# Performance work log

Hardware: AMD Instinct MI355X
Metric: run time of the kernel (lower is better)

Reference implementation:

```python
import jax, jax.numpy as jnp
import numpy as np

N = 100000          # nodes
E = 1600000         # edges (avg degree 16)
IN_DIM = 32
HID = 64
K = 2
XH = IN_DIM + HID   # 96, DiffConv input dim


def _xavier(key, shape):
    fan_in, fan_out = shape[-2], shape[-1]
    lim = float(np.sqrt(6.0 / (fan_in + fan_out)))
    return jax.random.uniform(key, shape, jnp.float32, -lim, lim)


def setup_inputs() -> dict:
    key = jax.random.key(0)
    ks = jax.random.split(key, 8)
    x = jax.random.normal(ks[0], (N, IN_DIM), jnp.float32)
    h = jax.random.normal(ks[1], (N, HID), jnp.float32)
    edge_index = jax.random.randint(ks[2], (2, E), 0, N, dtype=jnp.int32)
    edge_weight = jax.random.uniform(ks[3], (E,), jnp.float32)
    # stacked per-hop linear weights for each gate: (K+1, XH, HID)
    Wr = _xavier(ks[4], (K + 1, XH, HID))
    Wz = _xavier(ks[5], (K + 1, XH, HID))
    Wc = _xavier(ks[6], (K + 1, XH, HID))
    br = jnp.zeros((HID,), jnp.float32)
    bz = jnp.zeros((HID,), jnp.float32)
    bc = jnp.zeros((HID,), jnp.float32)
    return {"x": x, "h": h, "edge_index": edge_index, "edge_weight": edge_weight,
            "Wr": Wr, "br": br, "Wz": Wz, "bz": bz, "Wc": Wc, "bc": bc}


def _diff_conv(x, src, dst, norm_w, W, b, n):
    # DC(X) = sum_k Linear_k(P^k X),  P = D^{-1} W (row-normalised)
    out = x @ W[0]
    x_k = x
    for k in range(1, W.shape[0]):
        msgs = norm_w[:, None] * x_k[src]                     # gather + scale (E, F)
        x_k = jax.ops.segment_sum(msgs, dst, num_segments=n)  # scatter-add (N, F)
        out = out + x_k @ W[k]
    return out + b


def reference(x, h, edge_index, edge_weight, Wr, br, Wz, bz, Wc, bc):
    n = x.shape[0]
    src, dst = edge_index[0], edge_index[1]
    # out-degree normalisation on source nodes (clamped at 1)
    out_deg = jax.ops.segment_sum(jnp.ones_like(edge_weight), src, num_segments=n)
    out_deg = jnp.maximum(out_deg, 1.0)
    norm_w = edge_weight / out_deg[src]
    xh = jnp.concatenate([x, h], axis=-1)
    r = jax.nn.sigmoid(_diff_conv(xh, src, dst, norm_w, Wr, br, n))
    z = jax.nn.sigmoid(_diff_conv(xh, src, dst, norm_w, Wz, bz, n))
    xrh = jnp.concatenate([x, r * h], axis=-1)
    c = jnp.tanh(_diff_conv(xrh, src, dst, norm_w, Wc, bc, n))
    return z * h + (1.0 - z) * c
```

## Files before the change

### kernel.cpp

```cpp
#include <hip/hip_runtime.h>
#include <math.h>

#define NN 100000
#define NE 1600000
#define ECAP 64
#define GN 64
#define WSTR 296
#define LSTR 104

#define EPB 4096
#define NBLKA 391
#define BINB 256
#define NBINS 391
#define BCAP 4736

typedef __attribute__((ext_vector_type(4))) float f32x4;
typedef __attribute__((ext_vector_type(8))) short s16x8;

__device__ __forceinline__ unsigned int bfbits(float v) {
  unsigned int b = __float_as_uint(v);
  b += 0x7fffu + ((b >> 16) & 1u);
  return b >> 16;
}
__device__ __forceinline__ float bflo(unsigned int v) { return __uint_as_float(v << 16); }
__device__ __forceinline__ float bfhi(unsigned int v) { return __uint_as_float(v & 0xffff0000u); }
__device__ __forceinline__ float bf1(unsigned short v) { return __uint_as_float((unsigned int)v << 16); }

__global__ __launch_bounds__(256) void k_binA(const int* __restrict__ src,
                                              const int* __restrict__ dst,
                                              const float* __restrict__ ew,
                                              int* __restrict__ gcur1,
                                              int* __restrict__ gcur2,
                                              int2* __restrict__ rec1,
                                              unsigned char* __restrict__ rec2) {
  __shared__ int h1[NBINS], h2[NBINS];
  int tid = threadIdx.x;
  for (int t = tid; t < NBINS; t += 256) { h1[t] = 0; h2[t] = 0; }
  __syncthreads();
  int base = blockIdx.x * EPB;
  int end = base + EPB; if (end > NE) end = NE;
  for (int e = base + tid; e < end; e += 256) {
    atomicAdd(&h1[dst[e] >> 8], 1);
    atomicAdd(&h2[src[e] >> 8], 1);
  }
  __syncthreads();
  for (int t = tid; t < NBINS; t += 256) {
    int c1 = h1[t];
    h1[t] = t * BCAP + (c1 ? atomicAdd(&gcur1[t], c1) : 0);
    int c2 = h2[t];
    h2[t] = t * BCAP + (c2 ? atomicAdd(&gcur2[t], c2) : 0);
  }
  __syncthreads();
  for (int e = base + tid; e < end; e += 256) {
    int d = dst[e], s = src[e];
    int p1 = atomicAdd(&h1[d >> 8], 1);
    rec1[p1] = make_int2(s | ((d & 255) << 20), __float_as_int(ew[e]));
    int p2 = atomicAdd(&h2[s >> 8], 1);
    rec2[p2] = (unsigned char)(s & 255);
  }
}

__global__ __launch_bounds__(256) void k_bdeg(const int* __restrict__ gcur2,
                                              const unsigned char* __restrict__ rec2,
                                              int* __restrict__ deg_out) {
  __shared__ int lc[BINB];
  int b = blockIdx.x, tid = threadIdx.x;
  lc[tid] = 0;
  __syncthreads();
  int cnt = gcur2[b];
  const unsigned char* rp = rec2 + (size_t)b * BCAP;
  for (int i = tid; i < cnt; i += 256) atomicAdd(&lc[rp[i]], 1);
  __syncthreads();
  int node = b * 256 + tid;
  if (node < NN) deg_out[node] = lc[tid];
}

__global__ __launch_bounds__(256) void k_bell(const int* __restrict__ gcur1,
                                              const int2* __restrict__ rec1,
                                              const int* __restrict__ deg_out,
                                              int2* __restrict__ ell,
                                              int* __restrict__ cursor) {
  __shared__ int lc[BINB];
  int b = blockIdx.x, tid = threadIdx.x;
  lc[tid] = 0;
  __syncthreads();
  int cnt = gcur1[b];
  const int2* rp = rec1 + (size_t)b * BCAP;
  for (int i = tid; i < cnt; i += 256) {
    int2 r = rp[i];
    int s = r.x & 0xFFFFF;
    int dl = (r.x >> 20) & 255;
    float w = __int_as_float(r.y) / fmaxf((float)deg_out[s], 1.0f);
    int p = atomicAdd(&lc[dl], 1);
    if (p < ECAP)
      ell[(size_t)(b * 256 + dl) * ECAP + p] = make_int2(s, __float_as_int(w));
  }
  __syncthreads();
  int node = b * 256 + tid;
  if (node < NN) cursor[node] = lc[tid];
}

__global__ __launch_bounds__(256) void k_xh0(const float* __restrict__ x,
                                             const float* __restrict__ h,
                                             unsigned int* __restrict__ xh0) {
  int idx = blockIdx.x * 256 + threadIdx.x;
  if (idx >= NN * 48) return;
  int n = idx / 48, c = idx - n * 48;
  float v0, v1;
  if (c < 16) {
    v0 = x[(size_t)n * 32 + 2 * c];
    v1 = x[(size_t)n * 32 + 2 * c + 1];
  } else {
    v0 = h[(size_t)n * 64 + 2 * (c - 16)];
    v1 = h[(size_t)n * 64 + 2 * (c - 16) + 1];
  }
  xh0[idx] = bfbits(v0) | (bfbits(v1) << 16);
}

__global__ __launch_bounds__(256) void k_wprep(const float* __restrict__ Wr,
                                               const float* __restrict__ Wz,
                                               const float* __restrict__ Wc,
                                               unsigned short* __restrict__ wt_rz,
                                               unsigned short* __restrict__ wt_c) {
  int idx = blockIdx.x * 256 + threadIdx.x;
  if (idx >= 192 * 36) return;
  int col = idx % 192;
  int k0 = (idx / 192) * 8;
  unsigned int packed[4];
#pragma unroll
  for (int p = 0; p < 4; ++p) {
    unsigned int lo, hi;
#pragma unroll
    for (int e = 0; e < 2; ++e) {
      int k = k0 + p * 2 + e;
      int t = k / 96, kl = k - t * 96;
      float v;
      if (col < 64) v = Wr[t * 6144 + kl * 64 + col];
      else if (col < 128) v = Wz[t * 6144 + kl * 64 + (col - 64)];
      else v = Wc[t * 6144 + kl * 64 + (col - 128)];
      if (e == 0) lo = bfbits(v); else hi = bfbits(v);
    }
    packed[p] = lo | (hi << 16);
  }
  unsigned short* dstp = (col < 128) ? (wt_rz + col * WSTR + k0)
                                     : (wt_c + (col - 128) * WSTR + k0);
  *reinterpret_cast<uint4*>(dstp) =
      make_uint4(packed[0], packed[1], packed[2], packed[3]);
}

__global__ __launch_bounds__(256) void k_prop96e(const uint2* __restrict__ in,
                                                 uint2* __restrict__ out,
                                                 const int* __restrict__ cnt_arr,
                                                 const int2* __restrict__ ell) {
  int hw = (blockIdx.x * 256 + threadIdx.x) >> 5;
  int lane = threadIdx.x & 31;
  if (hw >= NN) return;
  int cnt = cnt_arr[hw];
  if (cnt > ECAP) cnt = ECAP;
  const int2* ep = ell + (size_t)hw * ECAP;
  bool act = lane < 24;
  float a0 = 0.f, a1 = 0.f, a2 = 0.f, a3 = 0.f;
  float b0 = 0.f, b1 = 0.f, b2 = 0.f, b3 = 0.f;
  int i = 0;
  for (; i + 4 <= cnt; i += 4) {
    int2 e0 = ep[i], e1 = ep[i + 1], e2 = ep[i + 2], e3 = ep[i + 3];
    if (act) {
      uint2 v0 = in[(size_t)e0.x * 24 + lane];
      uint2 v1 = in[(size_t)e1.x * 24 + lane];
      uint2 v2 = in[(size_t)e2.x * 24 + lane];
      uint2 v3 = in[(size_t)e3.x * 24 + lane];
      float w0 = __int_as_float(e0.y), w1 = __int_as_float(e1.y);
      float w2 = __int_as_float(e2.y), w3 = __int_as_float(e3.y);
      a0 = fmaf(w0, bflo(v0.x), a0); a1 = fmaf(w0, bfhi(v0.x), a1);
      a2 = fmaf(w0, bflo(v0.y), a2); a3 = fmaf(w0, bfhi(v0.y), a3);
      b0 = fmaf(w1, bflo(v1.x), b0); b1 = fmaf(w1, bfhi(v1.x), b1);
      b2 = fmaf(w1, bflo(v1.y), b2); b3 = fmaf(w1, bfhi(v1.y), b3);
      a0 = fmaf(w2, bflo(v2.x), a0); a1 = fmaf(w2, bfhi(v2.x), a1);
      a2 = fmaf(w2, bflo(v2.y), a2); a3 = fmaf(w2, bfhi(v2.y), a3);
      b0 = fmaf(w3, bflo(v3.x), b0); b1 = fmaf(w3, bfhi(v3.x), b1);
      b2 = fmaf(w3, bflo(v3.y), b2); b3 = fmaf(w3, bfhi(v3.y), b3);
    }
  }
  for (; i < cnt; ++i) {
    int2 e = ep[i];
    if (act) {
      uint2 v = in[(size_t)e.x * 24 + lane];
      float w = __int_as_float(e.y);
      a0 = fmaf(w, bflo(v.x), a0); a1 = fmaf(w, bfhi(v.x), a1);
      a2 = fmaf(w, bflo(v.y), a2); a3 = fmaf(w, bfhi(v.y), a3);
    }
  }
  if (act) {
    uint2 o;
    o.x = bfbits(a0 + b0) | (bfbits(a1 + b1) << 16);
    o.y = bfbits(a2 + b2) | (bfbits(a3 + b3) << 16);
    out[(size_t)hw * 24 + lane] = o;
  }
}

__global__ __launch_bounds__(256) void k_prop64e(const unsigned int* __restrict__ in,
                                                 unsigned int* __restrict__ out,
                                                 const int* __restrict__ cnt_arr,
                                                 const int2* __restrict__ ell) {
  int hw = (blockIdx.x * 256 + threadIdx.x) >> 5;
  int lane = threadIdx.x & 31;
  if (hw >= NN) return;
  int cnt = cnt_arr[hw];
  if (cnt > ECAP) cnt = ECAP;
  const int2* ep = ell + (size_t)hw * ECAP;
  float a0 = 0.f, a1 = 0.f, b0 = 0.f, b1 = 0.f;
  int i = 0;
  for (; i + 4 <= cnt; i += 4) {
    int2 e0 = ep[i], e1 = ep[i + 1], e2 = ep[i + 2], e3 = ep[i + 3];
    unsigned int v0 = in[(size_t)e0.x * 32 + lane];
    unsigned int v1 = in[(size_t)e1.x * 32 + lane];
    unsigned int v2 = in[(size_t)e2.x * 32 + lane];
    unsigned int v3 = in[(size_t)e3.x * 32 + lane];
    float w0 = __int_as_float(e0.y), w1 = __int_as_float(e1.y);
    float w2 = __int_as_float(e2.y), w3 = __int_as_float(e3.y);
    a0 = fmaf(w0, bflo(v0), a0); a1 = fmaf(w0, bfhi(v0), a1);
    b0 = fmaf(w1, bflo(v1), b0); b1 = fmaf(w1, bfhi(v1), b1);
    a0 = fmaf(w2, bflo(v2), a0); a1 = fmaf(w2, bfhi(v2), a1);
    b0 = fmaf(w3, bflo(v3), b0); b1 = fmaf(w3, bfhi(v3), b1);
  }
  for (; i < cnt; ++i) {
    int2 e = ep[i];
    unsigned int v = in[(size_t)e.x * 32 + lane];
    float w = __int_as_float(e.y);
    a0 = fmaf(w, bflo(v), a0); a1 = fmaf(w, bfhi(v), a1);
  }
  out[(size_t)hw * 32 + lane] = bfbits(a0 + b0) | (bfbits(a1 + b1) << 16);
}

__device__ __forceinline__ void stage_copy96(unsigned short* sA, int nb0,
                                             const unsigned short* __restrict__ src) {
  for (int i = threadIdx.x; i < GN * 12; i += 256) {
    int n = i / 12, ch = i % 12;
    int g = nb0 + n;
    uint4 v = make_uint4(0, 0, 0, 0);
    if (g < NN) v = *reinterpret_cast<const uint4*>(src + (size_t)g * 96 + ch * 8);
    *reinterpret_cast<uint4*>(&sA[n * LSTR + ch * 8]) = v;
  }
}

__device__ __forceinline__ void stage_bfbf(unsigned short* sA, int nb0,
                                           const unsigned short* __restrict__ srcA,
                                           const unsigned short* __restrict__ srcB) {
  for (int i = threadIdx.x; i < GN * 12; i += 256) {
    int n = i / 12, ch = i % 12;
    int g = nb0 + n;
    uint4 v = make_uint4(0, 0, 0, 0);
    if (g < NN) {
      if (ch < 4) v = *reinterpret_cast<const uint4*>(srcA + (size_t)g * 96 + ch * 8);
      else v = *reinterpret_cast<const uint4*>(srcB + (size_t)g * 64 + (ch - 4) * 8);
    }
    *reinterpret_cast<uint4*>(&sA[n * LSTR + ch * 8]) = v;
  }
}

__global__ __launch_bounds__(256) void k_rz(const unsigned short* __restrict__ xh0,
                                            const unsigned short* __restrict__ xh1,
                                            const unsigned short* __restrict__ xh2,
                                            const unsigned short* __restrict__ wt_rz,
                                            const float* __restrict__ br,
                                            const float* __restrict__ bz,
                                            unsigned short* __restrict__ rh,
                                            unsigned short* __restrict__ zbb) {
  __shared__ alignas(16) unsigned short sA[GN * LSTR];
  int tid = threadIdx.x;
  int nb0 = blockIdx.x * GN;
  int wv = tid >> 6, l = tid & 63;
  int l15 = l & 15, lg = l >> 4;
  int n0 = wv * 32;

  f32x4 acc[4][2];
#pragma unroll
  for (int nt = 0; nt < 2; ++nt) {
    int colc = n0 + nt * 16 + l15;
    float bias = (colc < 64) ? br[colc] : bz[colc - 64];
#pragma unroll
    for (int mt = 0; mt < 4; ++mt) acc[mt][nt] = {bias, bias, bias, bias};
  }

  const unsigned short* w0p = wt_rz + (size_t)(n0 + l15) * WSTR + lg * 8;
  const unsigned short* w1p = wt_rz + (size_t)(n0 + 16 + l15) * WSTR + lg * 8;

#pragma unroll
  for (int t = 0; t < 3; ++t) {
    if (t == 0) stage_copy96(sA, nb0, xh0);
    else if (t == 1) stage_copy96(sA, nb0, xh1);
    else stage_copy96(sA, nb0, xh2);
    __syncthreads();
#pragma unroll
    for (int ks = 0; ks < 3; ++ks) {
      int kb = ks * 32 + lg * 8;
      s16x8 bf0 = *reinterpret_cast<const s16x8*>(w0p + t * 96 + ks * 32);
      s16x8 bf1 = *reinterpret_cast<const s16x8*>(w1p + t * 96 + ks * 32);
#pragma unroll
      for (int mt = 0; mt < 4; ++mt) {
        s16x8 af = *reinterpret_cast<const s16x8*>(&sA[(mt * 16 + l15) * LSTR + kb]);
        acc[mt][0] = __builtin_amdgcn_mfma_f32_16x16x32_bf16(af, bf0, acc[mt][0], 0, 0, 0);
        acc[mt][1] = __builtin_amdgcn_mfma_f32_16x16x32_bf16(af, bf1, acc[mt][1], 0, 0, 0);
      }
    }
    __syncthreads();
  }

#pragma unroll
  for (int mt = 0; mt < 4; ++mt) {
#pragma unroll
    for (int nt = 0; nt < 2; ++nt) {
      int colc = n0 + nt * 16 + l15;
#pragma unroll
      for (int r = 0; r < 4; ++r) {
        int g = nb0 + mt * 16 + lg * 4 + r;
        if (g < NN) {
          float pre = acc[mt][nt][r];
          float sg = 1.f / (1.f + expf(-pre));
          if (colc < 64) {
            float hv = bf1(xh0[(size_t)g * 96 + 32 + colc]);
            rh[(size_t)g * 64 + colc] = (unsigned short)bfbits(sg * hv);
          } else {
            zbb[(size_t)g * 64 + (colc - 64)] = (unsigned short)bfbits(sg);
          }
        }
      }
    }
  }
}

__global__ __launch_bounds__(256) void k_c(const unsigned short* __restrict__ xh0,
                                           const unsigned short* __restrict__ rhf,
                                           const unsigned short* __restrict__ xh1,
                                           const unsigned short* __restrict__ xh2,
                                           const unsigned short* __restrict__ rh1,
                                           const unsigned short* __restrict__ rh2,
                                           const unsigned short* __restrict__ wt_c,
                                           const float* __restrict__ bc,
                                           const unsigned short* __restrict__ zbb,
                                           float* __restrict__ out) {
  __shared__ alignas(16) unsigned short sA[GN * LSTR];
  int tid = threadIdx.x;
  int nb0 = blockIdx.x * GN;
  int wv = tid >> 6, l = tid & 63;
  int l15 = l & 15, lg = l >> 4;
  int n0 = wv * 16;

  float bias = bc[n0 + l15];
  f32x4 acc[4];
#pragma unroll
  for (int mt = 0; mt < 4; ++mt) acc[mt] = {bias, bias, bias, bias};

  const unsigned short* wp = wt_c + (size_t)(n0 + l15) * WSTR + lg * 8;

#pragma unroll
  for (int t = 0; t < 3; ++t) {
    if (t == 0) stage_bfbf(sA, nb0, xh0, rhf);
    else if (t == 1) stage_bfbf(sA, nb0, xh1, rh1);
    else stage_bfbf(sA, nb0, xh2, rh2);
    __syncthreads();
#pragma unroll
    for (int ks = 0; ks < 3; ++ks) {
      int kb = ks * 32 + lg * 8;
      s16x8 bf0 = *reinterpret_cast<const s16x8*>(wp + t * 96 + ks * 32);
#pragma unroll
      for (int mt = 0; mt < 4; ++mt) {
        s16x8 af = *reinterpret_cast<const s16x8*>(&sA[(mt * 16 + l15) * LSTR + kb]);
        acc[mt] = __builtin_amdgcn_mfma_f32_16x16x32_bf16(af, bf0, acc[mt], 0, 0, 0);
      }
    }
    __syncthreads();
  }

  int colc = n0 + l15;
#pragma unroll
  for (int mt = 0; mt < 4; ++mt) {
#pragma unroll
    for (int r = 0; r < 4; ++r) {
      int g = nb0 + mt * 16 + lg * 4 + r;
      if (g < NN) {
        float cv = tanhf(acc[mt][r]);
        float z = bf1(zbb[(size_t)g * 64 + colc]);
        float hv = bf1(xh0[(size_t)g * 96 + 32 + colc]);
        out[(size_t)g * 64 + colc] = z * hv + (1.f - z) * cv;
      }
    }
  }
}

extern "C" void kernel_launch(void* const* d_in, const int* in_sizes, int n_in,
                              void* d_out, int out_size, void* d_ws, size_t ws_size,
                              hipStream_t stream) {
  const float* x = (const float*)d_in[0];
  const float* h = (const float*)d_in[1];
  const int* eidx = (const int*)d_in[2];
  const float* ew = (const float*)d_in[3];
  const float* Wr = (const float*)d_in[4];
  const float* br = (const float*)d_in[5];
  const float* Wz = (const float*)d_in[6];
  const float* bz = (const float*)d_in[7];
  const float* Wc = (const float*)d_in[8];
  const float* bc = (const float*)d_in[9];
  const int* src = eidx;
  const int* dst = eidx + NE;
  float* out = (float*)d_out;

  int* ip = (int*)d_ws;
  int* gcur1 = ip;
  int* gcur2 = ip + 512;
  int* deg_out = ip + 1024;
  int* cursor = deg_out + NN;
  int2* rec1 = (int2*)(cursor + NN);
  unsigned char* rec2 = (unsigned char*)(rec1 + (size_t)NBINS * BCAP);
  int2* ell = (int2*)(rec2 + ((size_t)NBINS * BCAP + 8) / 8 * 8);
  unsigned short* zbb = (unsigned short*)(ell + (size_t)NN * ECAP);
  unsigned short* xh0 = zbb + (size_t)NN * 64;
  unsigned short* xh1 = xh0 + (size_t)NN * 96;
  unsigned short* xh2 = xh1 + (size_t)NN * 96;
  unsigned short* rh  = xh2 + (size_t)NN * 96;
  unsigned short* rh1 = rh + (size_t)NN * 64;
  unsigned short* rh2 = rh1 + (size_t)NN * 64;
  unsigned short* wt_rz = rh2 + (size_t)NN * 64;
  unsigned short* wt_c = wt_rz + 128 * WSTR;

  hipMemsetAsync(ip, 0, 1024 * sizeof(int), stream);

  dim3 blk(256);
  k_wprep<<<dim3((192 * 36 + 255) / 256), blk, 0, stream>>>(Wr, Wz, Wc, wt_rz, wt_c);
  k_binA<<<dim3(NBLKA), blk, 0, stream>>>(src, dst, ew, gcur1, gcur2, rec1, rec2);
  k_bdeg<<<dim3(NBINS), blk, 0, stream>>>(gcur2, rec2, deg_out);
  k_bell<<<dim3(NBINS), blk, 0, stream>>>(gcur1, rec1, deg_out, ell, cursor);
  k_xh0<<<dim3(NN * 48 / 256), blk, 0, stream>>>(x, h, (unsigned int*)xh0);

  k_prop96e<<<dim3(NN / 8), blk, 0, stream>>>((const uint2*)xh0, (uint2*)xh1,
                                              cursor, ell);
  k_prop96e<<<dim3(NN / 8), blk, 0, stream>>>((const uint2*)xh1, (uint2*)xh2,
                                              cursor, ell);
  k_rz<<<dim3((NN + GN - 1) / GN), blk, 0, stream>>>(xh0, xh1, xh2, wt_rz, br, bz, rh, zbb);
  k_prop64e<<<dim3(NN / 8), blk, 0, stream>>>((const unsigned int*)rh,
                                              (unsigned int*)rh1, cursor, ell);
  k_prop64e<<<dim3(NN / 8), blk, 0, stream>>>((const unsigned int*)rh1,
                                              (unsigned int*)rh2, cursor, ell);
  k_c<<<dim3((NN + GN - 1) / GN), blk, 0, stream>>>(xh0, rh, xh1, xh2, rh1, rh2,
                                                    wt_c, bc, zbb, out);
}
```

Baseline: 387.5 us.

## Partition edge binning by bin group and use nontemporal ELL loads and stores

The binning kernel now processes 8192-edge chunks across 4 bin-group blocks. Each block only counts and scatters edges whose bin falls in its quarter of the bins, so every block writes to a narrower range of output regions and runs fewer global atomics per bin. The cost is that each edge chunk is read four times. The propagation kernels now read ELL edge records and write outputs with nontemporal loads and stores, meant to keep the gathered feature rows resident in cache.

```diff
diff --git a/kernel.cpp b/kernel.cpp
--- a/kernel.cpp
+++ b/kernel.cpp
@@ -8,8 +8,10 @@
 #define WSTR 296
 #define LSTR 104
 
-#define EPB 4096
-#define NBLKA 391
+#define EPB 8192
+#define NCHK 196
+#define BGRP 4
+#define BPG 98
 #define BINB 256
 #define NBINS 391
 #define BCAP 4736
@@ -33,30 +35,40 @@
                                               int* __restrict__ gcur2,
                                               int2* __restrict__ rec1,
                                               unsigned char* __restrict__ rec2) {
-  __shared__ int h1[NBINS], h2[NBINS];
+  __shared__ int h1[BPG], h2[BPG];
   int tid = threadIdx.x;
-  for (int t = tid; t < NBINS; t += 256) { h1[t] = 0; h2[t] = 0; }
-  __syncthreads();
-  int base = blockIdx.x * EPB;
+  int bg = blockIdx.x & (BGRP - 1);
+  int chunk = blockIdx.x >> 2;
+  int lo = bg * BPG;
+  int hi = lo + BPG; if (hi > NBINS) hi = NBINS;
+  for (int t = tid; t < BPG; t += 256) { h1[t] = 0; h2[t] = 0; }
+  __syncthreads();
+  int base = chunk * EPB;
   int end = base + EPB; if (end > NE) end = NE;
   for (int e = base + tid; e < end; e += 256) {
-    atomicAdd(&h1[dst[e] >> 8], 1);
-    atomicAdd(&h2[src[e] >> 8], 1);
-  }
-  __syncthreads();
-  for (int t = tid; t < NBINS; t += 256) {
+    int db = dst[e] >> 8, sb = src[e] >> 8;
+    if (db >= lo && db < hi) atomicAdd(&h1[db - lo], 1);
+    if (sb >= lo && sb < hi) atomicAdd(&h2[sb - lo], 1);
+  }
+  __syncthreads();
+  for (int t = tid; t < hi - lo; t += 256) {
     int c1 = h1[t];
-    h1[t] = t * BCAP + (c1 ? atomicAdd(&gcur1[t], c1) : 0);
+    h1[t] = (lo + t) * BCAP + (c1 ? atomicAdd(&gcur1[lo + t], c1) : 0);
     int c2 = h2[t];
-    h2[t] = t * BCAP + (c2 ? atomicAdd(&gcur2[t], c2) : 0);
+    h2[t] = (lo + t) * BCAP + (c2 ? atomicAdd(&gcur2[lo + t], c2) : 0);
   }
   __syncthreads();
   for (int e = base + tid; e < end; e += 256) {
     int d = dst[e], s = src[e];
-    int p1 = atomicAdd(&h1[d >> 8], 1);
-    rec1[p1] = make_int2(s | ((d & 255) << 20), __float_as_int(ew[e]));
-    int p2 = atomicAdd(&h2[s >> 8], 1);
-    rec2[p2] = (unsigned char)(s & 255);
+    int db = d >> 8, sb = s >> 8;
+    if (db >= lo && db < hi) {
+      int p1 = atomicAdd(&h1[db - lo], 1);
+      rec1[p1] = make_int2(s | ((d & 255) << 20), __float_as_int(ew[e]));
+    }
+    if (sb >= lo && sb < hi) {
+      int p2 = atomicAdd(&h2[sb - lo], 1);
+      rec2[p2] = (unsigned char)(s & 255);
+    }
   }
 }
 
@@ -146,6 +158,11 @@
                                      : (wt_c + (col - 128) * WSTR + k0);
   *reinterpret_cast<uint4*>(dstp) =
       make_uint4(packed[0], packed[1], packed[2], packed[3]);
+}
+
+__device__ __forceinline__ int2 nt_rec(const int2* p) {
+  long long v = __builtin_nontemporal_load(reinterpret_cast<const long long*>(p));
+  return make_int2((int)(v & 0xffffffffll), (int)(v >> 32));
 }
 
 __global__ __launch_bounds__(256) void k_prop96e(const uint2* __restrict__ in,
@@ -163,7 +180,8 @@
   float b0 = 0.f, b1 = 0.f, b2 = 0.f, b3 = 0.f;
   int i = 0;
   for (; i + 4 <= cnt; i += 4) {
-    int2 e0 = ep[i], e1 = ep[i + 1], e2 = ep[i + 2], e3 = ep[i + 3];
+    int2 e0 = nt_rec(ep + i), e1 = nt_rec(ep + i + 1);
+    int2 e2 = nt_rec(ep + i + 2), e3 = nt_rec(ep + i + 3);
     if (act) {
       uint2 v0 = in[(size_t)e0.x * 24 + lane];
       uint2 v1 = in[(size_t)e1.x * 24 + lane];
@@ -182,7 +200,7 @@
     }
   }
   for (; i < cnt; ++i) {
-    int2 e = ep[i];
+    int2 e = nt_rec(ep + i);
     if (act) {
       uint2 v = in[(size_t)e.x * 24 + lane];
       float w = __int_as_float(e.y);
@@ -191,10 +209,11 @@
     }
   }
   if (act) {
-    uint2 o;
-    o.x = bfbits(a0 + b0) | (bfbits(a1 + b1) << 16);
-    o.y = bfbits(a2 + b2) | (bfbits(a3 + b3) << 16);
-    out[(size_t)hw * 24 + lane] = o;
+    unsigned long long o =
+        (unsigned long long)(bfbits(a0 + b0) | (bfbits(a1 + b1) << 16)) |
+        ((unsigned long long)(bfbits(a2 + b2) | (bfbits(a3 + b3) << 16)) << 32);
+    __builtin_nontemporal_store(o,
+        reinterpret_cast<unsigned long long*>(out + (size_t)hw * 24 + lane));
   }
 }
 
@@ -211,7 +230,8 @@
   float a0 = 0.f, a1 = 0.f, b0 = 0.f, b1 = 0.f;
   int i = 0;
   for (; i + 4 <= cnt; i += 4) {
-    int2 e0 = ep[i], e1 = ep[i + 1], e2 = ep[i + 2], e3 = ep[i + 3];
+    int2 e0 = nt_rec(ep + i), e1 = nt_rec(ep + i + 1);
+    int2 e2 = nt_rec(ep + i + 2), e3 = nt_rec(ep + i + 3);
     unsigned int v0 = in[(size_t)e0.x * 32 + lane];
     unsigned int v1 = in[(size_t)e1.x * 32 + lane];
     unsigned int v2 = in[(size_t)e2.x * 32 + lane];
@@ -224,12 +244,13 @@
     b0 = fmaf(w3, bflo(v3), b0); b1 = fmaf(w3, bfhi(v3), b1);
   }
   for (; i < cnt; ++i) {
-    int2 e = ep[i];
+    int2 e = nt_rec(ep + i);
     unsigned int v = in[(size_t)e.x * 32 + lane];
     float w = __int_as_float(e.y);
     a0 = fmaf(w, bflo(v), a0); a1 = fmaf(w, bfhi(v), a1);
   }
-  out[(size_t)hw * 32 + lane] = bfbits(a0 + b0) | (bfbits(a1 + b1) << 16);
+  __builtin_nontemporal_store(bfbits(a0 + b0) | (bfbits(a1 + b1) << 16),
+                              out + (size_t)hw * 32 + lane);
 }
 
 __device__ __forceinline__ void stage_copy96(unsigned short* sA, int nb0,
@@ -427,7 +448,7 @@
 
   dim3 blk(256);
   k_wprep<<<dim3((192 * 36 + 255) / 256), blk, 0, stream>>>(Wr, Wz, Wc, wt_rz, wt_c);
-  k_binA<<<dim3(NBLKA), blk, 0, stream>>>(src, dst, ew, gcur1, gcur2, rec1, rec2);
+  k_binA<<<dim3(NCHK * BGRP), blk, 0, stream>>>(src, dst, ew, gcur1, gcur2, rec1, rec2);
   k_bdeg<<<dim3(NBINS), blk, 0, stream>>>(gcur2, rec2, deg_out);
   k_bell<<<dim3(NBINS), blk, 0, stream>>>(gcur1, rec1, deg_out, ell, cursor);
   k_xh0<<<dim3(NN * 48 / 256), blk, 0, stream>>>(x, h, (unsigned int*)xh0);
```

Result: slower. 440.6 us (+13.7%).
